# Kernel tuning notes

Hardware: AMD Instinct MI355X
Metric: run time of the kernel (lower is better)

Reference implementation:

```python
import jax, jax.numpy as jnp
import numpy as np

N = 100000       # nodes
E = 3200000      # edges (avg degree 32)
NFEAT, NHID, NCLASS = 1433, 40, 7
DROPOUT_P = 0.5


def setup_inputs() -> dict:
    key = jax.random.key(0)
    ks = jax.random.split(key, 9)
    x = jax.random.normal(ks[0], (N, NFEAT), dtype=jnp.float32)
    src = jax.random.randint(ks[1], (E,), 0, N, dtype=jnp.int32)
    dst = jax.random.randint(ks[2], (E,), 0, N, dtype=jnp.int32)
    edge_weight = jax.random.uniform(ks[3], (E,), dtype=jnp.float32)
    W1 = jax.random.normal(ks[4], (NFEAT, NHID), dtype=jnp.float32) * 0.05
    b1 = jnp.zeros((NHID,), dtype=jnp.float32)
    W2 = jax.random.normal(ks[5], (NHID, NCLASS), dtype=jnp.float32) * 0.05
    b2 = jnp.zeros((NCLASS,), dtype=jnp.float32)
    dropout_mask_u = jax.random.uniform(ks[6], (N, NHID), dtype=jnp.float32)
    return {"x": x, "src": src, "dst": dst, "edge_weight": edge_weight,
            "W1": W1, "b1": b1, "W2": W2, "b2": b2,
            "dropout_mask_u": dropout_mask_u}


def _gcn_layer(h, W, b, src, dst, edge_weight, n_nodes):
    # GCNConv (pygcn style): out = spmm(adj, h @ W) + b
    support = h @ W                                   # [N, out]
    msg = support[src] * edge_weight[:, None]         # [E, out] gather + scale
    agg = jax.ops.segment_sum(msg, dst, num_segments=n_nodes)  # scatter-add
    return agg + b


def reference(x, src, dst, edge_weight, W1, b1, W2, b2, dropout_mask_u):
    n = x.shape[0]
    h = jax.nn.relu(_gcn_layer(x, W1, b1, src, dst, edge_weight, n))
    # F.dropout(p=0.5, training=True): keep-mask scaled by 1/(1-p)
    keep = (dropout_mask_u > DROPOUT_P).astype(h.dtype) / (1.0 - DROPOUT_P)
    h = h * keep
    h = _gcn_layer(h, W2, b2, src, dst, edge_weight, n)
    return jax.nn.log_softmax(h, axis=1)
```

## Files before the change

### kernel.cpp

```cpp
#include <hip/hip_runtime.h>
#include <math.h>

#define N_NODES 100000
#define N_EDGES 3200000
#define NFEAT   1433
#define NHID    40
#define NCLASS  7
#define NCHUNK  391

__global__ __launch_bounds__(256) void k_hist(const int* __restrict__ dst, int* __restrict__ deg) {
    int e = blockIdx.x * 256 + threadIdx.x;
    if (e < N_EDGES) atomicAdd(&deg[dst[e]], 1);
}

__global__ __launch_bounds__(256) void k_scan1(const int* __restrict__ deg, int* __restrict__ csum) {
    __shared__ int s[256];
    int tid = threadIdx.x;
    int n = blockIdx.x * 256 + tid;
    int v = (n < N_NODES) ? deg[n] : 0;
    s[tid] = v; __syncthreads();
    for (int off = 128; off > 0; off >>= 1) {
        if (tid < off) s[tid] += s[tid + off];
        __syncthreads();
    }
    if (tid == 0) csum[blockIdx.x] = s[0];
}

__global__ __launch_bounds__(512) void k_scan2(int* __restrict__ csum) {
    __shared__ int s[512];
    int tid = threadIdx.x;
    int v = (tid < NCHUNK) ? csum[tid] : 0;
    s[tid] = v; __syncthreads();
    for (int off = 1; off < 512; off <<= 1) {
        int t = (tid >= off) ? s[tid - off] : 0;
        __syncthreads();
        s[tid] += t;
        __syncthreads();
    }
    if (tid < NCHUNK) csum[tid] = s[tid] - v;
}

__global__ __launch_bounds__(256) void k_scan3(const int* __restrict__ deg, const int* __restrict__ csum,
                                               int* __restrict__ row_ptr, int* __restrict__ cursor) {
    __shared__ int s[256];
    int tid = threadIdx.x;
    int n = blockIdx.x * 256 + tid;
    int v = (n < N_NODES) ? deg[n] : 0;
    s[tid] = v; __syncthreads();
    for (int off = 1; off < 256; off <<= 1) {
        int t = (tid >= off) ? s[tid - off] : 0;
        __syncthreads();
        s[tid] += t;
        __syncthreads();
    }
    int excl = s[tid] - v + csum[blockIdx.x];
    if (n < N_NODES) { row_ptr[n] = excl; cursor[n] = excl; }
    if (n == 0) row_ptr[N_NODES] = N_EDGES;
}

__global__ __launch_bounds__(256) void k_scatter(const int* __restrict__ src, const int* __restrict__ dst,
                                                 const float* __restrict__ ew, int* __restrict__ cursor,
                                                 int2* __restrict__ csr) {
    int e = blockIdx.x * 256 + threadIdx.x;
    if (e < N_EDGES) {
        int d = dst[e];
        int pos = atomicAdd(&cursor[d], 1);
        int2 p; p.x = src[e]; p.y = __float_as_int(ew[e]);
        csr[pos] = p;
    }
}

__global__ __launch_bounds__(256) void k_gemm1(const float* __restrict__ x,
                                               const float* __restrict__ W1,
                                               float* __restrict__ sup1) {
    __shared__ float xs[128 * 36];
    __shared__ float wsT[40 * 36];
    const int tid = threadIdx.x;
    const int colgrp = tid & 3;
    const int rowid = tid >> 2;
    const int row0 = blockIdx.x * 128;
    float acc[2][10];
#pragma unroll
    for (int j = 0; j < 2; ++j)
#pragma unroll
        for (int c = 0; c < 10; ++c) acc[j][c] = 0.f;

    for (int k0 = 0; k0 < NFEAT; k0 += 32) {
#pragma unroll
        for (int it = 0; it < 16; ++it) {
            int flat = it * 256 + tid;
            int r = flat >> 5, kk = flat & 31;
            int grow = row0 + r; if (grow >= N_NODES) grow = N_NODES - 1;
            int gk = k0 + kk;
            xs[r * 36 + kk] = (gk < NFEAT) ? x[(size_t)grow * NFEAT + gk] : 0.f;
        }
#pragma unroll
        for (int it = 0; it < 5; ++it) {
            int flat = it * 256 + tid;
            int k = flat / 40, c = flat - k * 40;
            int gk = k0 + k;
            wsT[c * 36 + k] = (gk < NFEAT) ? W1[(size_t)gk * NHID + c] : 0.f;
        }
        __syncthreads();
#pragma unroll
        for (int kk = 0; kk < 32; kk += 4) {
            float4 xv0 = *(const float4*)(xs + rowid * 36 + kk);
            float4 xv1 = *(const float4*)(xs + (rowid + 64) * 36 + kk);
#pragma unroll
            for (int c = 0; c < 10; ++c) {
                float4 wv = *(const float4*)(wsT + (colgrp * 10 + c) * 36 + kk);
                acc[0][c] += xv0.x * wv.x + xv0.y * wv.y + xv0.z * wv.z + xv0.w * wv.w;
                acc[1][c] += xv1.x * wv.x + xv1.y * wv.y + xv1.z * wv.z + xv1.w * wv.w;
            }
        }
        __syncthreads();
    }
#pragma unroll
    for (int j = 0; j < 2; ++j) {
        int row = row0 + rowid + 64 * j;
        if (row < N_NODES) {
            float* dp = sup1 + (size_t)row * NHID + colgrp * 10;
#pragma unroll
            for (int c = 0; c < 10; ++c) dp[c] = acc[j][c];
        }
    }
}

__global__ __launch_bounds__(256) void k_agg1(const float* __restrict__ sup1,
                                              const int* __restrict__ row_ptr,
                                              const int2* __restrict__ csr,
                                              const float* __restrict__ b1,
                                              const float* __restrict__ mask,
                                              float* __restrict__ h) {
    int wave = threadIdx.x >> 6;
    int lane = threadIdx.x & 63;
    int n = blockIdx.x * 4 + wave;
    if (n >= N_NODES) return;
    int start = row_ptr[n], end = row_ptr[n + 1];
    int half = lane >> 5, hl = lane & 31;
    float4 acc = make_float4(0.f, 0.f, 0.f, 0.f);
    for (int e = start + half; e < end; e += 2) {
        int2 p = csr[e];
        float w = __int_as_float(p.y);
        if (hl < 10) {
            float4 v = *(const float4*)(sup1 + (size_t)p.x * NHID + hl * 4);
            acc.x += w * v.x; acc.y += w * v.y; acc.z += w * v.z; acc.w += w * v.w;
        }
    }
    acc.x += __shfl_xor(acc.x, 32);
    acc.y += __shfl_xor(acc.y, 32);
    acc.z += __shfl_xor(acc.z, 32);
    acc.w += __shfl_xor(acc.w, 32);
    if (half == 0 && hl < 10) {
        float4 bb = *(const float4*)(b1 + hl * 4);
        const float* mp = mask + (size_t)n * NHID + hl * 4;
        float4 r;
        r.x = fmaxf(acc.x + bb.x, 0.f) * (mp[0] > 0.5f ? 2.f : 0.f);
        r.y = fmaxf(acc.y + bb.y, 0.f) * (mp[1] > 0.5f ? 2.f : 0.f);
        r.z = fmaxf(acc.z + bb.z, 0.f) * (mp[2] > 0.5f ? 2.f : 0.f);
        r.w = fmaxf(acc.w + bb.w, 0.f) * (mp[3] > 0.5f ? 2.f : 0.f);
        *(float4*)(h + (size_t)n * NHID + hl * 4) = r;
    }
}

__global__ __launch_bounds__(256) void k_gemm2(const float* __restrict__ h,
                                               const float* __restrict__ W2,
                                               float* __restrict__ sup2) {
    __shared__ float hs[256 * 42];
    __shared__ float w2s[NHID * NCLASS];
    const int tid = threadIdx.x;
    const int n0 = blockIdx.x * 256;
    for (int i = tid; i < NHID * NCLASS; i += 256) w2s[i] = W2[i];
#pragma unroll
    for (int it = 0; it < 20; ++it) {
        int flat = it * 256 + tid;
        int r = flat / 20, q = flat - r * 20;
        int grow = n0 + r; if (grow >= N_NODES) grow = N_NODES - 1;
        float2 v = *(const float2*)(h + (size_t)grow * NHID + q * 2);
        *(float2*)(hs + r * 42 + q * 2) = v;
    }
    __syncthreads();
    int n = n0 + tid;
    float acc[NCLASS];
#pragma unroll
    for (int c = 0; c < NCLASS; ++c) acc[c] = 0.f;
#pragma unroll
    for (int k = 0; k < NHID; ++k) {
        float hv = hs[tid * 42 + k];
#pragma unroll
        for (int c = 0; c < NCLASS; ++c) acc[c] += hv * w2s[k * NCLASS + c];
    }
    if (n < N_NODES) {
        float* dp = sup2 + (size_t)n * NCLASS;
#pragma unroll
        for (int c = 0; c < NCLASS; ++c) dp[c] = acc[c];
    }
}

__global__ __launch_bounds__(256) void k_agg2(const float* __restrict__ sup2,
                                              const int* __restrict__ row_ptr,
                                              const int2* __restrict__ csr,
                                              const float* __restrict__ b2,
                                              float* __restrict__ out) {
    int wave = threadIdx.x >> 6;
    int lane = threadIdx.x & 63;
    int n = blockIdx.x * 4 + wave;
    if (n >= N_NODES) return;
    int start = row_ptr[n], end = row_ptr[n + 1];
    int g = lane >> 3, f = lane & 7;
    float acc = 0.f;
    for (int base = start; base < end; base += 8) {
        int e = base + g;
        if (e < end) {
            int2 p = csr[e];
            if (f < NCLASS) acc += __int_as_float(p.y) * sup2[(size_t)p.x * NCLASS + f];
        }
    }
    acc += __shfl_xor(acc, 8);
    acc += __shfl_xor(acc, 16);
    acc += __shfl_xor(acc, 32);
    float v = (f < NCLASS) ? acc + b2[f] : -INFINITY;
    float m = v;
    m = fmaxf(m, __shfl_xor(m, 1));
    m = fmaxf(m, __shfl_xor(m, 2));
    m = fmaxf(m, __shfl_xor(m, 4));
    float ex = expf(v - m);
    float s = ex;
    s += __shfl_xor(s, 1);
    s += __shfl_xor(s, 2);
    s += __shfl_xor(s, 4);
    if (g == 0 && f < NCLASS) out[(size_t)n * NCLASS + f] = v - m - logf(s);
}

extern "C" void kernel_launch(void* const* d_in, const int* in_sizes, int n_in,
                              void* d_out, int out_size, void* d_ws, size_t ws_size,
                              hipStream_t stream) {
    const float* x    = (const float*)d_in[0];
    const int*   src  = (const int*)d_in[1];
    const int*   dst  = (const int*)d_in[2];
    const float* ew   = (const float*)d_in[3];
    const float* W1   = (const float*)d_in[4];
    const float* b1   = (const float*)d_in[5];
    const float* W2   = (const float*)d_in[6];
    const float* b2   = (const float*)d_in[7];
    const float* mask = (const float*)d_in[8];
    float* out = (float*)d_out;

    char* ws = (char*)d_ws;
    float* sup1   = (float*)(ws + 0);
    float* h      = (float*)(ws + 16000000);
    float* sup2   = (float*)(ws + 32000000);
    int* row_ptr  = (int*)(ws + 34800000);
    int* cursor   = (int*)(ws + 35200016);
    int* deg      = (int*)(ws + 35600016);
    int* csum     = (int*)(ws + 36000016);
    int2* csr     = (int2*)(ws + 36001584);

    hipMemsetAsync(deg, 0, N_NODES * sizeof(int), stream);
    k_hist   <<<(N_EDGES + 255) / 256, 256, 0, stream>>>(dst, deg);
    k_scan1  <<<NCHUNK, 256, 0, stream>>>(deg, csum);
    k_scan2  <<<1, 512, 0, stream>>>(csum);
    k_scan3  <<<NCHUNK, 256, 0, stream>>>(deg, csum, row_ptr, cursor);
    k_scatter<<<(N_EDGES + 255) / 256, 256, 0, stream>>>(src, dst, ew, cursor, csr);
    k_gemm1  <<<(N_NODES + 127) / 128, 256, 0, stream>>>(x, W1, sup1);
    k_agg1   <<<N_NODES / 4, 256, 0, stream>>>(sup1, row_ptr, csr, b1, mask, h);
    k_gemm2  <<<(N_NODES + 255) / 256, 256, 0, stream>>>(h, W2, sup2);
    k_agg2   <<<N_NODES / 4, 256, 0, stream>>>(sup2, row_ptr, csr, b2, out);
}
```

Before: 2.532 ms.

## Double-buffer GEMM1 tiles with direct global-to-LDS loads and swizzled layout

Rewrites the x·W1 GEMM main loop to double-buffer both the x tile and the W1 tile in shared memory. The next tile is fetched while the current one is computed: x goes through global_load_lds straight into LDS, and W1 is prefetched into registers. The x tile drops its padded stride in favour of an XOR swizzle to avoid LDS bank conflicts. Bounds handling now clamps indices instead of zero-filling, which relies on the zero-padded W1 rows to cancel the out-of-range x values. It also relies on the barrier waiting for the async LDS loads to land.

Result: no change. 2.495 ms (-1.5%).

```diff
diff --git a/kernel.cpp b/kernel.cpp
--- a/kernel.cpp
+++ b/kernel.cpp
@@ -7,6 +7,7 @@
 #define NHID    40
 #define NCLASS  7
 #define NCHUNK  391
+#define GTILE   45
 
 __global__ __launch_bounds__(256) void k_hist(const int* __restrict__ dst, int* __restrict__ deg) {
     int e = blockIdx.x * 256 + threadIdx.x;
@@ -70,51 +71,128 @@
     }
 }
 
+
+__device__ __forceinline__ void gl_lds4(const float* g, float* l) {
+    __builtin_amdgcn_global_load_lds(
+        (const __attribute__((address_space(1))) void*)g,
+        (__attribute__((address_space(3))) void*)l, 4, 0, 0);
+}
+
 __global__ __launch_bounds__(256) void k_gemm1(const float* __restrict__ x,
                                                const float* __restrict__ W1,
                                                float* __restrict__ sup1) {
-    __shared__ float xs[128 * 36];
-    __shared__ float wsT[40 * 36];
+    __shared__ float xsA[128 * 32];
+    __shared__ float xsB[128 * 32];
+    __shared__ float wsA[40 * 36];
+    __shared__ float wsB[40 * 36];
+
     const int tid = threadIdx.x;
+    const int lane = tid & 63;
+    const int wave = tid >> 6;
     const int colgrp = tid & 3;
     const int rowid = tid >> 2;
     const int row0 = blockIdx.x * 128;
+    const int xorv = (rowid & 7) << 2;
+
+    const int r_lane = wave * 32 + (lane >> 5);
+    const int klin = lane & 31;
+    int klx[4];
+#pragma unroll
+    for (int m = 0; m < 4; ++m)
+        klx[m] = klin ^ ((((lane >> 5) + 2 * m) & 7) << 2);
+
+    int waddr[5];
+#pragma unroll
+    for (int it = 0; it < 5; ++it) {
+        int flat = it * 256 + tid;
+        int k = flat / 40, c = flat - k * 40;
+        waddr[it] = c * 36 + k;
+    }
+
+    float wr[5];
     float acc[2][10];
 #pragma unroll
     for (int j = 0; j < 2; ++j)
 #pragma unroll
         for (int c = 0; c < 10; ++c) acc[j][c] = 0.f;
 
-    for (int k0 = 0; k0 < NFEAT; k0 += 32) {
-#pragma unroll
-        for (int it = 0; it < 16; ++it) {
-            int flat = it * 256 + tid;
-            int r = flat >> 5, kk = flat & 31;
-            int grow = row0 + r; if (grow >= N_NODES) grow = N_NODES - 1;
-            int gk = k0 + kk;
-            xs[r * 36 + kk] = (gk < NFEAT) ? x[(size_t)grow * NFEAT + gk] : 0.f;
-        }
-#pragma unroll
-        for (int it = 0; it < 5; ++it) {
-            int flat = it * 256 + tid;
-            int k = flat / 40, c = flat - k * 40;
-            int gk = k0 + k;
-            wsT[c * 36 + k] = (gk < NFEAT) ? W1[(size_t)gk * NHID + c] : 0.f;
-        }
-        __syncthreads();
-#pragma unroll
-        for (int kk = 0; kk < 32; kk += 4) {
-            float4 xv0 = *(const float4*)(xs + rowid * 36 + kk);
-            float4 xv1 = *(const float4*)(xs + (rowid + 64) * 36 + kk);
-#pragma unroll
-            for (int c = 0; c < 10; ++c) {
-                float4 wv = *(const float4*)(wsT + (colgrp * 10 + c) * 36 + kk);
-                acc[0][c] += xv0.x * wv.x + xv0.y * wv.y + xv0.z * wv.z + xv0.w * wv.w;
-                acc[1][c] += xv1.x * wv.x + xv1.y * wv.y + xv1.z * wv.z + xv1.w * wv.w;
-            }
-        }
-        __syncthreads();
-    }
+#define STAGE_X(t, XB)                                                    \
+    {                                                                     \
+        const int k0_ = (t) * 32;                                         \
+        _Pragma("unroll")                                                 \
+        for (int i = 0; i < 16; ++i) {                                    \
+            int row_ = row0 + r_lane + 2 * i;                             \
+            if (row_ > N_NODES - 1) row_ = N_NODES - 1;                   \
+            int gk_ = k0_ + klx[i & 3];                                   \
+            if (gk_ > NFEAT - 1) gk_ = NFEAT - 1;                         \
+            gl_lds4(x + (size_t)row_ * NFEAT + gk_,                       \
+                    (XB) + wave * 1024 + i * 64);                         \
+        }                                                                 \
+    }
+
+#define LOADW(t)                                                          \
+    {                                                                     \
+        const int base_ = (t) * 32 * NHID + tid;                          \
+        _Pragma("unroll")                                                 \
+        for (int it = 0; it < 5; ++it) {                                  \
+            int idx_ = base_ + it * 256;                                  \
+            wr[it] = (idx_ < NFEAT * NHID) ? W1[idx_] : 0.f;              \
+        }                                                                 \
+    }
+
+#define WRITEW(WB)                                                        \
+    {                                                                     \
+        _Pragma("unroll")                                                 \
+        for (int it = 0; it < 5; ++it) (WB)[waddr[it]] = wr[it];          \
+    }
+
+#define COMPUTE(XB, WB)                                                   \
+    {                                                                     \
+        const float* xb_ = (XB) + rowid * 32;                             \
+        const float* wb_ = (WB) + colgrp * 360;                           \
+        _Pragma("unroll")                                                 \
+        for (int kk = 0; kk < 32; kk += 4) {                              \
+            int xo_ = kk ^ xorv;                                          \
+            float4 xv0 = *(const float4*)(xb_ + xo_);                     \
+            float4 xv1 = *(const float4*)(xb_ + xo_ + 2048);              \
+            _Pragma("unroll")                                             \
+            for (int c = 0; c < 10; ++c) {                                \
+                float4 wv = *(const float4*)(wb_ + c * 36 + kk);          \
+                acc[0][c] += xv0.x * wv.x + xv0.y * wv.y +                \
+                             xv0.z * wv.z + xv0.w * wv.w;                 \
+                acc[1][c] += xv1.x * wv.x + xv1.y * wv.y +                \
+                             xv1.z * wv.z + xv1.w * wv.w;                 \
+            }                                                             \
+        }                                                                 \
+    }
+
+#define ITER(t, CX, CW, NX, NW)                                           \
+    {                                                                     \
+        LOADW((t) + 1);                                                   \
+        STAGE_X((t) + 1, NX);                                             \
+        __builtin_amdgcn_sched_barrier(0);                                \
+        COMPUTE(CX, CW);                                                  \
+        WRITEW(NW);                                                       \
+        __syncthreads();                                                  \
+    }
+
+    LOADW(0);
+    STAGE_X(0, xsA);
+    WRITEW(wsA);
+    __syncthreads();
+
+    for (int t = 0; t < GTILE - 1; t += 2) {
+        ITER(t,     xsA, wsA, xsB, wsB);
+        ITER(t + 1, xsB, wsB, xsA, wsA);
+    }
+    COMPUTE(xsA, wsA);
+
+#undef STAGE_X
+#undef LOADW
+#undef WRITEW
+#undef COMPUTE
+#undef ITER
+
 #pragma unroll
     for (int j = 0; j < 2; ++j) {
         int row = row0 + rowid + 64 * j;
```
